# Optimization experiments

Hardware: AMD Instinct MI355X
Metric: run time of the kernel (lower is better)

## Reference

```python
import jax, jax.numpy as jnp
import numpy as np

N = 50000
E = 800000
HID = 128
FILT = 128
NG = 50
CUTOFF = 10.0
LOG2 = float(np.log(2.0))


def shifted_softplus(x):
    return jax.nn.softplus(x) - LOG2


def setup_inputs() -> dict:
    key = jax.random.key(0)
    ks = jax.random.split(key, 12)
    s_hid = 1.0 / np.sqrt(HID)
    s_ng = 1.0 / np.sqrt(NG)
    s_f = 1.0 / np.sqrt(FILT)
    return {
        "h": jax.random.normal(ks[0], (N, HID), jnp.float32),
        "pos": jax.random.normal(ks[1], (N, 3), jnp.float32),
        "edge_index": jax.random.randint(ks[2], (2, E), 0, N, jnp.int64),
        # edge filter MLP: Linear(NG->FILT), ssp, Linear(FILT->FILT)
        "mlp_w1": jax.random.uniform(ks[3], (NG, FILT), jnp.float32, -s_ng, s_ng),
        "mlp_b1": jax.random.uniform(ks[4], (FILT,), jnp.float32, -s_ng, s_ng),
        "mlp_w2": jax.random.uniform(ks[5], (FILT, FILT), jnp.float32, -s_f, s_f),
        "mlp_b2": jax.random.uniform(ks[6], (FILT,), jnp.float32, -s_f, s_f),
        # CFConv lin1 (no bias), lin2
        "lin1_w": jax.random.uniform(ks[7], (HID, FILT), jnp.float32, -s_hid, s_hid),
        "lin2_w": jax.random.uniform(ks[8], (FILT, HID), jnp.float32, -s_f, s_f),
        "lin2_b": jax.random.uniform(ks[9], (HID,), jnp.float32, -s_f, s_f),
        # InteractionBlock output linear
        "lin_w": jax.random.uniform(ks[10], (HID, HID), jnp.float32, -s_hid, s_hid),
        "lin_b": jax.random.uniform(ks[11], (HID,), jnp.float32, -s_hid, s_hid),
    }


def reference(h, pos, edge_index, mlp_w1, mlp_b1, mlp_w2, mlp_b2,
              lin1_w, lin2_w, lin2_b, lin_w, lin_b):
    row, col = edge_index[0], edge_index[1]  # target, source (PyG convention)

    # edge distances  [E]
    edge_weight = jnp.linalg.norm(pos[row] - pos[col], axis=-1)

    # GaussianSmearing: offsets linspace(0, cutoff, NG)  -> [E, NG]
    offset = jnp.linspace(0.0, CUTOFF, NG, dtype=h.dtype)
    coeff = -0.5 / (offset[1] - offset[0]) ** 2
    edge_attr = jnp.exp(coeff * (edge_weight[:, None] - offset) ** 2)

    # CFConv: cosine cutoff * filter MLP   -> edge filters W [E, FILT]
    C = 0.5 * (jnp.cos(edge_weight * (jnp.pi / CUTOFF)) + 1.0)
    W = shifted_softplus(edge_attr @ mlp_w1 + mlp_b1) @ mlp_w2 + mlp_b2
    W = W * C[:, None]

    # gather-modulate-scatter message passing
    x = h @ lin1_w                    # [N, FILT]
    msg = x[col] * W                  # [E, FILT]
    agg = jax.ops.segment_sum(msg, row, num_segments=N)  # [N, FILT]
    x = agg @ lin2_w + lin2_b         # [N, HID]

    # InteractionBlock tail
    x = shifted_softplus(x)
    x = x @ lin_w + lin_b
    return x
```

## Files before the change

### kernel.cpp

```cpp
#include <hip/hip_runtime.h>
#include <hip/hip_bf16.h>
#include <math.h>

#define HID   128
#define NG    50
#define TN    8192
#define TMAXD 16.0f
#define RPB   8
#define TSPB  16
#define TBLB  512
#define NRG   16
#define NSL   32
#define SCAN_CHUNK 1024

typedef __attribute__((ext_vector_type(8))) short bf16x8;
typedef __attribute__((ext_vector_type(4))) float f32x4;
typedef __attribute__((ext_vector_type(4))) int   i32x4;
typedef unsigned short u16;
typedef unsigned int   u32;

#define LOG2F 0.69314718056f

__device__ __forceinline__ float sspf(float v) {
    if (v > 15.f) return v - LOG2F;
    return __logf(1.f + __expf(v)) - LOG2F;
}

__device__ __forceinline__ u16 f2bf(float f) {
    __hip_bfloat16 h = __float2bfloat16(f);
    return *reinterpret_cast<u16*>(&h);
}
__device__ __forceinline__ float bf2f(u32 v) {
    union { u32 u; float f; } x; x.u = v << 16; return x.f;
}

union K1Smem {
    struct { float sattr[TSPB][64]; float st1[TSPB][128]; } tb;
    int hcnt[3328];
};

__global__ __launch_bounds__(256) void k1_table_hist_prep(
    const float* __restrict__ w1, const float* __restrict__ b1,
    const float* __restrict__ w2, const float* __restrict__ b2,
    u16* __restrict__ Tn,
    const int* __restrict__ eidx, int* __restrict__ cntp,
    const float* __restrict__ lin1, const float* __restrict__ lin2,
    const float* __restrict__ linw,
    u16* __restrict__ lin1T, u16* __restrict__ lin2T, u16* __restrict__ linwT,
    int N, int E)
{
    __shared__ K1Smem sm;

    const int tid = threadIdx.x;
    const int b   = blockIdx.x;

    if (b < TBLB) {
        const int s0 = b * TSPB;
        const float TSTEP = TMAXD / TN;
        const float GSTEP = 10.0f / 49.0f;
        const float COEFF = -0.5f / (GSTEP * GSTEP);

        for (int idx = tid; idx < TSPB * 64; idx += 256) {
            int s = idx >> 6, g = idx & 63;
            float v = 0.f;
            if (g < NG) {
                float d = (float)(s0 + s) * TSTEP;
                float t = d - (float)g * GSTEP;
                v = __expf(COEFF * t * t);
            }
            sm.tb.sattr[s][g] = v;
        }
        __syncthreads();

        const int c  = tid & 127;
        const int sh = tid >> 7;

        for (int s = sh; s < TSPB; s += 2) {
            float acc = b1[c];
#pragma unroll
            for (int g = 0; g < NG; ++g)
                acc = fmaf(sm.tb.sattr[s][g], w1[g * 128 + c], acc);
            sm.tb.st1[s][c] = sspf(acc);
        }
        __syncthreads();

        for (int s = sh; s < TSPB; s += 2) {
            float acc = b2[c];
#pragma unroll 8
            for (int k = 0; k < 128; ++k)
                acc = fmaf(sm.tb.st1[s][k], w2[k * 128 + c], acc);
            float d = (float)(s0 + s) * TSTEP;
            float Cf = 0.5f * (__cosf(d * 0.31415926535f) + 1.0f);
            Tn[(size_t)(s0 + s) * HID + c] = f2bf(acc * Cf);
        }
    } else if (b < TBLB + NRG * NSL) {
        int* hcnt = sm.hcnt;
        const int hb  = b - TBLB;
        const int rg  = hb / NSL;
        const int sl  = hb % NSL;
        const int rph = (N + NRG - 1) / NRG;
        const int lo  = rg * rph;
        const int hi  = min(lo + rph, N);
        const int nr  = hi - lo;

        for (int i = tid; i < nr; i += 256) hcnt[i] = 0;
        __syncthreads();

        const int esz = (E / NSL) & ~3;
        const int es  = sl * esz;
        const int ee  = (sl == NSL - 1) ? E : es + esz;
        const int n4  = (ee - es) >> 2;
        const i32x4* p4 = reinterpret_cast<const i32x4*>(eidx + es);
        for (int i = tid; i < n4; i += 256) {
            i32x4 v = p4[i];
#pragma unroll
            for (int j = 0; j < 4; ++j) {
                u32 rr = (u32)(v[j] - lo);
                if (rr < (u32)nr) atomicAdd(&hcnt[rr], 1);
            }
        }
        for (int e = es + (n4 << 2) + tid; e < ee; e += 256) {
            u32 rr = (u32)(eidx[e] - lo);
            if (rr < (u32)nr) atomicAdd(&hcnt[rr], 1);
        }
        __syncthreads();

        for (int i = tid; i < nr; i += 256)
            cntp[(size_t)sl * N + lo + i] = hcnt[i];
    } else {
        const int wt  = b - TBLB - NRG * NSL;
        const int wid = wt >> 6;
        const int t   = (wt & 63) * 256 + tid;
        const int n = t >> 7, k = t & 127;
        const float* src = (wid == 0) ? lin1 : (wid == 1) ? lin2 : linw;
        u16* dst = (wid == 0) ? lin1T : (wid == 1) ? lin2T : linwT;
        dst[t] = f2bf(src[k * 128 + n]);
    }
}

__global__ __launch_bounds__(256) void k2_part_mfma(
    const int* __restrict__ cntp, int* __restrict__ cnt, int* __restrict__ part,
    int nch,
    const float* __restrict__ h, const u16* __restrict__ lin1T,
    u16* __restrict__ bx, int N)
{
    __shared__ u16 sA[64 * 128];
    __shared__ int red[256];
    const int tid = threadIdx.x;

    if ((int)blockIdx.x < nch) {
        const int b = blockIdx.x;
        int base = b * SCAN_CHUNK + tid * 4;
        int s = 0;
#pragma unroll
        for (int i = 0; i < 4; ++i) {
            int idx = base + i;
            if (idx < N) {
                int v = 0;
#pragma unroll
                for (int sl = 0; sl < NSL; ++sl)
                    v += cntp[(size_t)sl * N + idx];
                cnt[idx] = v;
                s += v;
            }
        }
        red[tid] = s;
        __syncthreads();
        for (int off = 128; off > 0; off >>= 1) {
            if (tid < off) red[tid] += red[tid + off];
            __syncthreads();
        }
        if (tid == 0) part[b] = red[0];
        return;
    }

    const int r0 = ((int)blockIdx.x - nch) * 64;

    for (int i = tid; i < 64 * 16; i += 256) {
        int row = i >> 4, ck = i & 15;
        i32x4 pk = (i32x4){0, 0, 0, 0};
        if (r0 + row < N) {
            const float* src = h + (size_t)(r0 + row) * HID + ck * 8;
            f32x4 a = *reinterpret_cast<const f32x4*>(src);
            f32x4 c = *reinterpret_cast<const f32x4*>(src + 4);
            pk[0] = (int)((u32)f2bf(a[0]) | ((u32)f2bf(a[1]) << 16));
            pk[1] = (int)((u32)f2bf(a[2]) | ((u32)f2bf(a[3]) << 16));
            pk[2] = (int)((u32)f2bf(c[0]) | ((u32)f2bf(c[1]) << 16));
            pk[3] = (int)((u32)f2bf(c[2]) | ((u32)f2bf(c[3]) << 16));
        }
        int byteoff = row * 256 + ((ck * 16) ^ ((row & 7) << 4));
        *reinterpret_cast<i32x4*>(reinterpret_cast<char*>(sA) + byteoff) = pk;
    }
    __syncthreads();

    const int lane = tid & 63;
    const int wv   = tid >> 6;
    const int l15  = lane & 15;
    const int l4   = lane >> 4;

    bf16x8 bw[2][4];
#pragma unroll
    for (int nt = 0; nt < 2; ++nt)
#pragma unroll
        for (int s = 0; s < 4; ++s) {
            int n = wv * 32 + nt * 16 + l15;
            bw[nt][s] = *reinterpret_cast<const bf16x8*>(lin1T + n * 128 + s * 32 + l4 * 8);
        }

    f32x4 acc[4][2];
#pragma unroll
    for (int mt = 0; mt < 4; ++mt) { acc[mt][0] = (f32x4){0,0,0,0}; acc[mt][1] = (f32x4){0,0,0,0}; }

#pragma unroll
    for (int mt = 0; mt < 4; ++mt)
#pragma unroll
        for (int s = 0; s < 4; ++s) {
            int e = mt * 16 + l15;
            int byteoff = e * 256 + ((s * 64 + l4 * 16) ^ ((e & 7) << 4));
            bf16x8 af = *reinterpret_cast<const bf16x8*>(reinterpret_cast<char*>(sA) + byteoff);
            acc[mt][0] = __builtin_amdgcn_mfma_f32_16x16x32_bf16(af, bw[0][s], acc[mt][0], 0, 0, 0);
            acc[mt][1] = __builtin_amdgcn_mfma_f32_16x16x32_bf16(af, bw[1][s], acc[mt][1], 0, 0, 0);
        }

#pragma unroll
    for (int mt = 0; mt < 4; ++mt)
#pragma unroll
        for (int nt = 0; nt < 2; ++nt)
#pragma unroll
            for (int r = 0; r < 4; ++r) {
                int row = r0 + mt * 16 + l4 * 4 + r;
                if (row < N)
                    bx[(size_t)row * HID + wv * 32 + nt * 16 + l15] = f2bf(acc[mt][nt][r]);
            }
}

__global__ __launch_bounds__(256) void scan_write(
    const int* __restrict__ cnt, const int* __restrict__ part,
    int* __restrict__ cur, int N)
{
    __shared__ int sc[256];
    int b = blockIdx.x, tid = threadIdx.x;
    int base = 0;
    for (int i = 0; i < b; ++i) base += part[i];
    int gbase = b * SCAN_CHUNK + tid * 4;
    int v[4];
#pragma unroll
    for (int i = 0; i < 4; ++i) { int idx = gbase + i; v[i] = (idx < N) ? cnt[idx] : 0; }
    int tsum = v[0] + v[1] + v[2] + v[3];
    sc[tid] = tsum;
    __syncthreads();
    for (int off = 1; off < 256; off <<= 1) {
        int add = (tid >= off) ? sc[tid - off] : 0;
        __syncthreads();
        sc[tid] += add;
        __syncthreads();
    }
    int tpre = base + sc[tid] - tsum;
    int run = 0;
#pragma unroll
    for (int i = 0; i < 4; ++i) {
        int idx = gbase + i;
        if (idx < N) cur[idx] = tpre + run;
        run += v[i];
    }
}

__global__ void scatter2(const int* __restrict__ eidx, const float* __restrict__ pos,
                         int* __restrict__ cur, u32* __restrict__ ec, int E)
{
    for (int e = blockIdx.x * 256 + threadIdx.x; e < E; e += gridDim.x * 256) {
        int r = eidx[e], c = eidx[E + e];
        float dx = pos[3 * r + 0] - pos[3 * c + 0];
        float dy = pos[3 * r + 1] - pos[3 * c + 1];
        float dz = pos[3 * r + 2] - pos[3 * c + 2];
        float d = sqrtf(dx * dx + dy * dy + dz * dz);
        int idx = (int)(d * (TN / TMAXD) + 0.5f);
        idx = min(idx, TN - 1);
        int p = atomicAdd(&cur[r], 1);
        ec[p] = ((u32)idx << 16) | (u32)c;
    }
}

__device__ __forceinline__ void eload4(
    const u32 v[4], const u16* __restrict__ Tn, const u16* __restrict__ bx,
    int c2, u32 T[4], u32 X[4])
{
#pragma unroll
    for (int j = 0; j < 4; ++j) {
        u32 rv = (u32)__builtin_amdgcn_readfirstlane((int)v[j]);
        int is = (int)(rv >> 16);
        int cs = (int)(rv & 0xffffu);
        T[j] = *reinterpret_cast<const u32*>(Tn + (size_t)is * HID + c2);
        X[j] = *reinterpret_cast<const u32*>(bx + (size_t)cs * HID + c2);
    }
}

__device__ __forceinline__ void efma4(
    const u32 T[4], const u32 X[4], float& ax, float& ay)
{
#pragma unroll
    for (int j = 0; j < 4; ++j) {
        ax = fmaf(bf2f(T[j] & 0xffffu), bf2f(X[j] & 0xffffu), ax);
        ay = fmaf(bf2f(T[j] >> 16), bf2f(X[j] >> 16), ay);
    }
}

__device__ __forceinline__ void eone(
    u32 v0, const u16* __restrict__ Tn, const u16* __restrict__ bx,
    int c2, float& ax, float& ay)
{
    u32 rv = (u32)__builtin_amdgcn_readfirstlane((int)v0);
    int is = (int)(rv >> 16);
    int cs = (int)(rv & 0xffffu);
    u32 T0 = *reinterpret_cast<const u32*>(Tn + (size_t)is * HID + c2);
    u32 X0 = *reinterpret_cast<const u32*>(bx + (size_t)cs * HID + c2);
    ax = fmaf(bf2f(T0 & 0xffffu), bf2f(X0 & 0xffffu), ax);
    ay = fmaf(bf2f(T0 >> 16), bf2f(X0 >> 16), ay);
}

__global__ __launch_bounds__(256) void edge_csr(
    const int* __restrict__ rowend,
    const u32* __restrict__ ec,
    const u16* __restrict__ Tn,
    const u16* __restrict__ bx,
    float*     __restrict__ agg,
    int N)
{
    const int lane = threadIdx.x & 63;
    const int slot = threadIdx.x >> 6;
    const int c2   = lane * 2;
    const int r0   = blockIdx.x * RPB;

    const int rA = r0 + slot;
    const int rB = r0 + 4 + slot;

    int eA = 0, eeA = 0, eB = 0, eeB = 0;
    if (rA < N) { eA = (rA == 0) ? 0 : rowend[rA - 1]; eeA = rowend[rA]; }
    if (rB < N) { eB = rowend[rB - 1]; eeB = rowend[rB]; }

    float axA = 0.f, ayA = 0.f, axB = 0.f, ayB = 0.f;
    u32 vA[4], vB[4];
    u32 TA[4], TB[4];
    u32 XA[4], XB[4];

    while (eA + 4 <= eeA && eB + 4 <= eeB) {
#pragma unroll
        for (int j = 0; j < 4; ++j) { vA[j] = ec[eA + j]; vB[j] = ec[eB + j]; }
        eload4(vA, Tn, bx, c2, TA, XA);
        eload4(vB, Tn, bx, c2, TB, XB);
        efma4(TA, XA, axA, ayA);
        efma4(TB, XB, axB, ayB);
        eA += 4; eB += 4;
    }
    while (eA + 4 <= eeA) {
#pragma unroll
        for (int j = 0; j < 4; ++j) vA[j] = ec[eA + j];
        eload4(vA, Tn, bx, c2, TA, XA);
        efma4(TA, XA, axA, ayA);
        eA += 4;
    }
    for (; eA < eeA; ++eA) eone(ec[eA], Tn, bx, c2, axA, ayA);
    while (eB + 4 <= eeB) {
#pragma unroll
        for (int j = 0; j < 4; ++j) vB[j] = ec[eB + j];
        eload4(vB, Tn, bx, c2, TB, XB);
        efma4(TB, XB, axB, ayB);
        eB += 4;
    }
    for (; eB < eeB; ++eB) eone(ec[eB], Tn, bx, c2, axB, ayB);

    if (rA < N) {
        float2 o; o.x = axA; o.y = ayA;
        *reinterpret_cast<float2*>(agg + (size_t)rA * HID + c2) = o;
    }
    if (rB < N) {
        float2 o; o.x = axB; o.y = ayB;
        *reinterpret_cast<float2*>(agg + (size_t)rB * HID + c2) = o;
    }
}

__global__ __launch_bounds__(256) void tail_mfma(
    const float* __restrict__ agg,
    const u16* __restrict__ lin2T, const float* __restrict__ l2b,
    const u16* __restrict__ linwT, const float* __restrict__ linb,
    float* __restrict__ out, int N)
{
    __shared__ u16 sA[64 * 128];
    __shared__ u16 sT[64 * 128];

    const int tid = threadIdx.x;
    const int r0 = blockIdx.x * 64;

    for (int i = tid; i < 64 * 16; i += 256) {
        int row = i >> 4, ck = i & 15;
        i32x4 pk = (i32x4){0, 0, 0, 0};
        if (r0 + row < N) {
            const float* src = agg + (size_t)(r0 + row) * HID + ck * 8;
            f32x4 a = *reinterpret_cast<const f32x4*>(src);
            f32x4 c = *reinterpret_cast<const f32x4*>(src + 4);
            pk[0] = (int)((u32)f2bf(a[0]) | ((u32)f2bf(a[1]) << 16));
            pk[1] = (int)((u32)f2bf(a[2]) | ((u32)f2bf(a[3]) << 16));
            pk[2] = (int)((u32)f2bf(c[0]) | ((u32)f2bf(c[1]) << 16));
            pk[3] = (int)((u32)f2bf(c[2]) | ((u32)f2bf(c[3]) << 16));
        }
        int byteoff = row * 256 + ((ck * 16) ^ ((row & 7) << 4));
        *reinterpret_cast<i32x4*>(reinterpret_cast<char*>(sA) + byteoff) = pk;
    }
    __syncthreads();

    const int lane = tid & 63;
    const int wv   = tid >> 6;
    const int l15  = lane & 15;
    const int l4   = lane >> 4;
    const int n0   = wv * 32 + l15;
    const int n1   = n0 + 16;

    {
        bf16x8 bw[2][4];
#pragma unroll
        for (int nt = 0; nt < 2; ++nt)
#pragma unroll
            for (int s = 0; s < 4; ++s) {
                int n = wv * 32 + nt * 16 + l15;
                bw[nt][s] = *reinterpret_cast<const bf16x8*>(lin2T + n * 128 + s * 32 + l4 * 8);
            }

        f32x4 acc[4][2];
#pragma unroll
        for (int mt = 0; mt < 4; ++mt) { acc[mt][0] = (f32x4){0,0,0,0}; acc[mt][1] = (f32x4){0,0,0,0}; }

#pragma unroll
        for (int mt = 0; mt < 4; ++mt)
#pragma unroll
            for (int s = 0; s < 4; ++s) {
                int e = mt * 16 + l15;
                int byteoff = e * 256 + ((s * 64 + l4 * 16) ^ ((e & 7) << 4));
                bf16x8 af = *reinterpret_cast<const bf16x8*>(reinterpret_cast<char*>(sA) + byteoff);
                acc[mt][0] = __builtin_amdgcn_mfma_f32_16x16x32_bf16(af, bw[0][s], acc[mt][0], 0, 0, 0);
                acc[mt][1] = __builtin_amdgcn_mfma_f32_16x16x32_bf16(af, bw[1][s], acc[mt][1], 0, 0, 0);
            }

        const float bb0 = l2b[n0];
        const float bb1 = l2b[n1];
#pragma unroll
        for (int mt = 0; mt < 4; ++mt)
#pragma unroll
            for (int nt = 0; nt < 2; ++nt) {
                const int n = (nt == 0) ? n0 : n1;
                const float bb = (nt == 0) ? bb0 : bb1;
#pragma unroll
                for (int r = 0; r < 4; ++r) {
                    int m = mt * 16 + l4 * 4 + r;
                    float v = sspf(acc[mt][nt][r] + bb);
                    int byteoff = m * 256 + ((n * 2) ^ ((m & 7) << 4));
                    *reinterpret_cast<u16*>(reinterpret_cast<char*>(sT) + byteoff) = f2bf(v);
                }
            }
    }
    __syncthreads();

    {
        bf16x8 bw[2][4];
#pragma unroll
        for (int nt = 0; nt < 2; ++nt)
#pragma unroll
            for (int s = 0; s < 4; ++s) {
                int n = wv * 32 + nt * 16 + l15;
                bw[nt][s] = *reinterpret_cast<const bf16x8*>(linwT + n * 128 + s * 32 + l4 * 8);
            }

        f32x4 acc[4][2];
#pragma unroll
        for (int mt = 0; mt < 4; ++mt) { acc[mt][0] = (f32x4){0,0,0,0}; acc[mt][1] = (f32x4){0,0,0,0}; }

#pragma unroll
        for (int mt = 0; mt < 4; ++mt)
#pragma unroll
            for (int s = 0; s < 4; ++s) {
                int e = mt * 16 + l15;
                int byteoff = e * 256 + ((s * 64 + l4 * 16) ^ ((e & 7) << 4));
                bf16x8 af = *reinterpret_cast<const bf16x8*>(reinterpret_cast<char*>(sT) + byteoff);
                acc[mt][0] = __builtin_amdgcn_mfma_f32_16x16x32_bf16(af, bw[0][s], acc[mt][0], 0, 0, 0);
                acc[mt][1] = __builtin_amdgcn_mfma_f32_16x16x32_bf16(af, bw[1][s], acc[mt][1], 0, 0, 0);
            }

        const float cb0 = linb[n0];
        const float cb1 = linb[n1];
#pragma unroll
        for (int mt = 0; mt < 4; ++mt)
#pragma unroll
            for (int nt = 0; nt < 2; ++nt) {
                const int n = (nt == 0) ? n0 : n1;
                const float cb = (nt == 0) ? cb0 : cb1;
#pragma unroll
                for (int r = 0; r < 4; ++r) {
                    int row = r0 + mt * 16 + l4 * 4 + r;
                    if (row < N)
                        out[(size_t)row * HID + n] = acc[mt][nt][r] + cb;
                }
            }
    }
}

extern "C" void kernel_launch(void* const* d_in, const int* in_sizes, int n_in,
                              void* d_out, int out_size, void* d_ws, size_t ws_size,
                              hipStream_t stream)
{
    const float* h    = (const float*)d_in[0];
    const float* pos  = (const float*)d_in[1];
    const int*   eidx = (const int*)  d_in[2];
    const float* w1   = (const float*)d_in[3];
    const float* b1   = (const float*)d_in[4];
    const float* w2   = (const float*)d_in[5];
    const float* b2   = (const float*)d_in[6];
    const float* lin1 = (const float*)d_in[7];
    const float* lin2 = (const float*)d_in[8];
    const float* l2b  = (const float*)d_in[9];
    const float* linw = (const float*)d_in[10];
    const float* linb = (const float*)d_in[11];

    const int N = in_sizes[0] / HID;
    const int E = in_sizes[2] / 2;

    char* ws = (char*)d_ws;
    size_t off = 0;
    auto alloc = [&](size_t bytes) { char* p = ws + off; off = (off + bytes + 255) & ~(size_t)255; return p; };

    u16*    bx    = (u16*)   alloc((size_t)N * HID * sizeof(u16));
    u16*    Tn    = (u16*)   alloc((size_t)TN * HID * sizeof(u16));
    float*  agg   = (float*) alloc((size_t)N * HID * sizeof(float));
    int*    cntp  = (int*)   alloc((size_t)NSL * N * sizeof(int));
    int*    cnt   = (int*)   alloc((size_t)N * sizeof(int));
    int*    cur   = (int*)   alloc((size_t)N * sizeof(int));
    int*    part  = (int*)   alloc(256 * sizeof(int));
    u32*    ec    = (u32*)   alloc(((size_t)E + 8) * sizeof(u32));
    u16*    lin1T = (u16*)   alloc(128 * 128 * sizeof(u16));
    u16*    lin2T = (u16*)   alloc(128 * 128 * sizeof(u16));
    u16*    linwT = (u16*)   alloc(128 * 128 * sizeof(u16));

    k1_table_hist_prep<<<TBLB + NRG * NSL + 192, 256, 0, stream>>>(
        w1, b1, w2, b2, Tn, eidx, cntp, lin1, lin2, linw, lin1T, lin2T, linwT, N, E);

    const int nch = (N + SCAN_CHUNK - 1) / SCAN_CHUNK;
    const int ngb = (N + 63) / 64;
    k2_part_mfma<<<nch + ngb, 256, 0, stream>>>(cntp, cnt, part, nch, h, lin1T, bx, N);

    scan_write<<<nch, 256, 0, stream>>>(cnt, part, cur, N);

    scatter2<<<1024, 256, 0, stream>>>(eidx, pos, cur, ec, E);

    edge_csr<<<(N + RPB - 1) / RPB, 256, 0, stream>>>(cur, ec, Tn, bx, agg, N);

    tail_mfma<<<ngb, 256, 0, stream>>>(agg, lin2T, l2b, linwT, linb, (float*)d_out, N);
}
```

Measured before the change: 151.4 us.

## Replace global-atomic edge scatter with per-slice LDS counting-sort scatter

Edge distance-index/column records are now computed in the first kernel into a temporary array. The old scatter did one global atomic per edge on a row cursor. It is replaced by a counting-sort scatter: k2 turns the per-slice histograms into exclusive per-slice offsets, and each (row-group, slice) block uses LDS atomics to place records at cursor+slice offset. This removes global atomic contention and also makes edge order within each row deterministic. The cost is an extra E-sized buffer, and every scatter block rereads its whole edge slice.

```diff
diff --git a/kernel.cpp b/kernel.cpp
--- a/kernel.cpp
+++ b/kernel.cpp
@@ -44,6 +44,7 @@
     const float* __restrict__ w2, const float* __restrict__ b2,
     u16* __restrict__ Tn,
     const int* __restrict__ eidx, int* __restrict__ cntp,
+    const float* __restrict__ pos, u32* __restrict__ rec,
     const float* __restrict__ lin1, const float* __restrict__ lin2,
     const float* __restrict__ linw,
     u16* __restrict__ lin1T, u16* __restrict__ lin2T, u16* __restrict__ linwT,
@@ -127,7 +128,7 @@
 
         for (int i = tid; i < nr; i += 256)
             cntp[(size_t)sl * N + lo + i] = hcnt[i];
-    } else {
+    } else if (b < TBLB + NRG * NSL + 192) {
         const int wt  = b - TBLB - NRG * NSL;
         const int wid = wt >> 6;
         const int t   = (wt & 63) * 256 + tid;
@@ -135,11 +136,24 @@
         const float* src = (wid == 0) ? lin1 : (wid == 1) ? lin2 : linw;
         u16* dst = (wid == 0) ? lin1T : (wid == 1) ? lin2T : linwT;
         dst[t] = f2bf(src[k * 128 + n]);
+    } else {
+        const int rb = b - TBLB - NRG * NSL - 192;
+        const int e  = rb * 256 + tid;
+        if (e < E) {
+            int r = eidx[e], c = eidx[E + e];
+            float dx = pos[3 * r + 0] - pos[3 * c + 0];
+            float dy = pos[3 * r + 1] - pos[3 * c + 1];
+            float dz = pos[3 * r + 2] - pos[3 * c + 2];
+            float d = sqrtf(dx * dx + dy * dy + dz * dz);
+            int idx = (int)(d * (TN / TMAXD) + 0.5f);
+            idx = min(idx, TN - 1);
+            rec[e] = ((u32)idx << 16) | (u32)c;
+        }
     }
 }
 
 __global__ __launch_bounds__(256) void k2_part_mfma(
-    const int* __restrict__ cntp, int* __restrict__ cnt, int* __restrict__ part,
+    int* __restrict__ cntp, int* __restrict__ cnt, int* __restrict__ part,
     int nch,
     const float* __restrict__ h, const u16* __restrict__ lin1T,
     u16* __restrict__ bx, int N)
@@ -156,12 +170,15 @@
         for (int i = 0; i < 4; ++i) {
             int idx = base + i;
             if (idx < N) {
-                int v = 0;
-#pragma unroll
-                for (int sl = 0; sl < NSL; ++sl)
-                    v += cntp[(size_t)sl * N + idx];
-                cnt[idx] = v;
-                s += v;
+                int run = 0;
+#pragma unroll
+                for (int sl = 0; sl < NSL; ++sl) {
+                    int v = cntp[(size_t)sl * N + idx];
+                    cntp[(size_t)sl * N + idx] = run;
+                    run += v;
+                }
+                cnt[idx] = run;
+                s += run;
             }
         }
         red[tid] = s;
@@ -265,19 +282,49 @@
     }
 }
 
-__global__ void scatter2(const int* __restrict__ eidx, const float* __restrict__ pos,
-                         int* __restrict__ cur, u32* __restrict__ ec, int E)
-{
-    for (int e = blockIdx.x * 256 + threadIdx.x; e < E; e += gridDim.x * 256) {
-        int r = eidx[e], c = eidx[E + e];
-        float dx = pos[3 * r + 0] - pos[3 * c + 0];
-        float dy = pos[3 * r + 1] - pos[3 * c + 1];
-        float dz = pos[3 * r + 2] - pos[3 * c + 2];
-        float d = sqrtf(dx * dx + dy * dy + dz * dz);
-        int idx = (int)(d * (TN / TMAXD) + 0.5f);
-        idx = min(idx, TN - 1);
-        int p = atomicAdd(&cur[r], 1);
-        ec[p] = ((u32)idx << 16) | (u32)c;
+__global__ __launch_bounds__(256) void scatter_sorted(
+    const int* __restrict__ eidx, const u32* __restrict__ rec,
+    const int* __restrict__ cur, const int* __restrict__ cntp,
+    u32* __restrict__ ec, int N, int E)
+{
+    __shared__ int lbase[3328];
+    __shared__ int lcnt[3328];
+    const int tid = threadIdx.x;
+    const int rg  = blockIdx.x / NSL;
+    const int sl  = blockIdx.x % NSL;
+    const int rph = (N + NRG - 1) / NRG;
+    const int lo  = rg * rph;
+    const int hi  = min(lo + rph, N);
+    const int nr  = hi - lo;
+
+    for (int i = tid; i < nr; i += 256) {
+        lbase[i] = cur[lo + i] + cntp[(size_t)sl * N + lo + i];
+        lcnt[i]  = 0;
+    }
+    __syncthreads();
+
+    const int esz = (E / NSL) & ~3;
+    const int es  = sl * esz;
+    const int ee  = (sl == NSL - 1) ? E : es + esz;
+    const int n4  = (ee - es) >> 2;
+    const i32x4* p4 = reinterpret_cast<const i32x4*>(eidx + es);
+    for (int i = tid; i < n4; i += 256) {
+        i32x4 v = p4[i];
+#pragma unroll
+        for (int j = 0; j < 4; ++j) {
+            u32 rr = (u32)(v[j] - lo);
+            if (rr < (u32)nr) {
+                int o = atomicAdd(&lcnt[rr], 1);
+                ec[lbase[rr] + o] = rec[es + (i << 2) + j];
+            }
+        }
+    }
+    for (int e = es + (n4 << 2) + tid; e < ee; e += 256) {
+        u32 rr = (u32)(eidx[e] - lo);
+        if (rr < (u32)nr) {
+            int o = atomicAdd(&lcnt[rr], 1);
+            ec[lbase[rr] + o] = rec[e];
+        }
     }
 }
 
@@ -319,12 +366,12 @@
 }
 
 __global__ __launch_bounds__(256) void edge_csr(
-    const int* __restrict__ rowend,
+    const int* __restrict__ rowstart,
     const u32* __restrict__ ec,
     const u16* __restrict__ Tn,
     const u16* __restrict__ bx,
     float*     __restrict__ agg,
-    int N)
+    int N, int E)
 {
     const int lane = threadIdx.x & 63;
     const int slot = threadIdx.x >> 6;
@@ -335,8 +382,8 @@
     const int rB = r0 + 4 + slot;
 
     int eA = 0, eeA = 0, eB = 0, eeB = 0;
-    if (rA < N) { eA = (rA == 0) ? 0 : rowend[rA - 1]; eeA = rowend[rA]; }
-    if (rB < N) { eB = rowend[rB - 1]; eeB = rowend[rB]; }
+    if (rA < N) { eA = rowstart[rA]; eeA = (rA == N - 1) ? E : rowstart[rA + 1]; }
+    if (rB < N) { eB = rowstart[rB]; eeB = (rB == N - 1) ? E : rowstart[rB + 1]; }
 
     float axA = 0.f, ayA = 0.f, axB = 0.f, ayB = 0.f;
     u32 vA[4], vB[4];
@@ -533,13 +580,17 @@
     int*    cnt   = (int*)   alloc((size_t)N * sizeof(int));
     int*    cur   = (int*)   alloc((size_t)N * sizeof(int));
     int*    part  = (int*)   alloc(256 * sizeof(int));
+    u32*    rec   = (u32*)   alloc((size_t)E * sizeof(u32));
     u32*    ec    = (u32*)   alloc(((size_t)E + 8) * sizeof(u32));
     u16*    lin1T = (u16*)   alloc(128 * 128 * sizeof(u16));
     u16*    lin2T = (u16*)   alloc(128 * 128 * sizeof(u16));
     u16*    linwT = (u16*)   alloc(128 * 128 * sizeof(u16));
 
-    k1_table_hist_prep<<<TBLB + NRG * NSL + 192, 256, 0, stream>>>(
-        w1, b1, w2, b2, Tn, eidx, cntp, lin1, lin2, linw, lin1T, lin2T, linwT, N, E);
+    const int nrec = (E + 255) / 256;
+
+    k1_table_hist_prep<<<TBLB + NRG * NSL + 192 + nrec, 256, 0, stream>>>(
+        w1, b1, w2, b2, Tn, eidx, cntp, pos, rec,
+        lin1, lin2, linw, lin1T, lin2T, linwT, N, E);
 
     const int nch = (N + SCAN_CHUNK - 1) / SCAN_CHUNK;
     const int ngb = (N + 63) / 64;
@@ -547,9 +598,9 @@
 
     scan_write<<<nch, 256, 0, stream>>>(cnt, part, cur, N);
 
-    scatter2<<<1024, 256, 0, stream>>>(eidx, pos, cur, ec, E);
-
-    edge_csr<<<(N + RPB - 1) / RPB, 256, 0, stream>>>(cur, ec, Tn, bx, agg, N);
+    scatter_sorted<<<NRG * NSL, 256, 0, stream>>>(eidx, rec, cur, cntp, ec, N, E);
+
+    edge_csr<<<(N + RPB - 1) / RPB, 256, 0, stream>>>(cur, ec, Tn, bx, agg, N, E);
 
     tail_mfma<<<ngb, 256, 0, stream>>>(agg, lin2T, l2b, linwT, linb, (float*)d_out, N);
 }
```

New measurement: 150.6 us (median of 3 runs). About the same (-0.5%).
